# Kernel tuning notes

Hardware: AMD Instinct MI355X
Metric: run time of the kernel (lower is better)

Reference implementation:

```python
import jax, jax.numpy as jnp
import numpy as np

NUM_HEADS = 16


def setup_inputs() -> dict:
    key = jax.random.key(0)
    ks = jax.random.split(key, 7)
    B, S, D = 2, 2048, 1024
    scale = 1.0 / np.sqrt(D)
    return {
        "queries": jax.random.normal(ks[0], (B, S, D), jnp.float32),
        "keys": jax.random.normal(ks[1], (B, S, D), jnp.float32),
        "values": jax.random.normal(ks[2], (B, S, D), jnp.float32),
        "Wq": jax.random.normal(ks[3], (D, D), jnp.float32) * scale,
        "Wk": jax.random.normal(ks[4], (D, D), jnp.float32) * scale,
        "Wv": jax.random.normal(ks[5], (D, D), jnp.float32) * scale,
        "Wo": jax.random.normal(ks[6], (D, D), jnp.float32) * scale,
    }


def _split_heads(x, h):
    # [B, S, D] -> [B, h, S, D/h]
    B, S, D = x.shape
    return x.reshape(B, S, h, D // h).transpose(0, 2, 1, 3)


def reference(queries, keys, values, Wq, Wk, Wv, Wo):
    h = NUM_HEADS
    q = _split_heads(queries @ Wq, h)  # [B, h, S, dh]
    k = _split_heads(keys @ Wk, h)
    v = _split_heads(values @ Wv, h)
    dh = q.shape[-1]
    scores = jnp.einsum("bhqd,bhkd->bhqk", q, k) / jnp.sqrt(jnp.float32(dh))
    attn = jax.nn.softmax(scores, axis=-1)
    y = jnp.einsum("bhqk,bhkd->bhqd", attn, v)  # [B, h, S, dh]
    B, _, S, _ = y.shape
    y = y.transpose(0, 2, 1, 3).reshape(B, S, h * dh)
    return y @ Wo
```

## Files before the change

### kernel.cpp

```cpp
#include <hip/hip_runtime.h>
#include <hip/hip_bf16.h>


typedef __attribute__((ext_vector_type(8))) short bf16x8;
typedef __attribute__((ext_vector_type(4))) float f32x4;
typedef __attribute__((ext_vector_type(16))) float f32x16;
typedef __attribute__((ext_vector_type(4))) unsigned int u32x4;

#define QSCALE 0.18033688011112042f

__device__ __forceinline__ unsigned short f2b(float f) {
    unsigned int u = __float_as_uint(f);
    u += 0x7FFFu + ((u >> 16) & 1u);
    return (unsigned short)(u >> 16);
}

__device__ __forceinline__ unsigned cvt_pk_bf16(float lo, float hi) {
    unsigned r;
    asm("v_cvt_pk_bf16_f32 %0, %1, %2" : "=v"(r) : "v"(lo), "v"(hi));
    return r;
}

__device__ __forceinline__ float exp2a(float x) {
    float r;
    asm("v_exp_f32 %0, %1\n\ts_nop 1" : "=v"(r) : "v"(x));
    return r;
}

__device__ __forceinline__ void gld_lds16(const void* g, void* l) {
    __builtin_amdgcn_global_load_lds(
        (const __attribute__((address_space(1))) unsigned int*)g,
        (__attribute__((address_space(3))) unsigned int*)l, 16, 0, 0);
}

__global__ __launch_bounds__(256) void f32_to_bf16_3(
    const float* __restrict__ i0, const float* __restrict__ i1, const float* __restrict__ i2,
    unsigned short* __restrict__ o0, unsigned short* __restrict__ o1, unsigned short* __restrict__ o2)
{
    const int z = blockIdx.y;
    const float* in = z == 0 ? i0 : (z == 1 ? i1 : i2);
    unsigned short* out = z == 0 ? o0 : (z == 1 ? o1 : o2);
    int i = blockIdx.x * 256 + threadIdx.x;
    float4 v = ((const float4*)in)[i];
    ushort4 o;
    o.x = f2b(v.x); o.y = f2b(v.y); o.z = f2b(v.z); o.w = f2b(v.w);
    ((ushort4*)out)[i] = o;
}

__global__ __launch_bounds__(256) void transpose_w4(
    const float* __restrict__ W0, const float* __restrict__ W1,
    const float* __restrict__ W2, const float* __restrict__ W3,
    unsigned short* __restrict__ O0, unsigned short* __restrict__ O1,
    unsigned short* __restrict__ O2, unsigned short* __restrict__ O3)
{
    __shared__ unsigned short tile[32][33];
    const int z = blockIdx.z;
    const float* in = z == 0 ? W0 : z == 1 ? W1 : z == 2 ? W2 : W3;
    unsigned short* out = z == 0 ? O0 : z == 1 ? O1 : z == 2 ? O2 : O3;
    const int c0 = blockIdx.x * 32, r0 = blockIdx.y * 32;
    const int tx = threadIdx.x, ty = threadIdx.y;
#pragma unroll
    for (int i = 0; i < 4; ++i)
        tile[ty + i * 8][tx] = f2b(in[(size_t)(r0 + ty + i * 8) * 1024 + c0 + tx]);
    __syncthreads();
#pragma unroll
    for (int i = 0; i < 4; ++i)
        out[(size_t)(c0 + ty + i * 8) * 1024 + r0 + tx] = tile[tx][ty + i * 8];
}

template <int BN, int MODE>
__global__ __launch_bounds__(256) void gemm_bt(
    const unsigned short* __restrict__ A0, const unsigned short* __restrict__ A1,
    const unsigned short* __restrict__ A2,
    const unsigned short* __restrict__ B0, const unsigned short* __restrict__ B1,
    const unsigned short* __restrict__ B2,
    void* __restrict__ Cq, void* __restrict__ Ck, void* __restrict__ Cv)
{
    constexpr int K = 1024, N = 1024;
    constexpr int NB = BN / 32;
    __shared__ unsigned short lds_a[128 * 32];
    __shared__ unsigned short lds_b[BN * 32];
    const int tid = threadIdx.x;
    const int wid = tid >> 6, ln = tid & 15, lg = (tid & 63) >> 4;
    const int z = (MODE == 1) ? blockIdx.z : 0;
    const unsigned short* A = (z == 0) ? A0 : (z == 1) ? A1 : A2;
    const unsigned short* Bt = (z == 0) ? B0 : (z == 1) ? B1 : B2;
    const int m0 = blockIdx.y * 128, n0 = blockIdx.x * BN;
    const int wr = wid >> 1, wc = wid & 1;

    f32x4 acc[4][NB];
#pragma unroll
    for (int m = 0; m < 4; ++m)
#pragma unroll
        for (int n = 0; n < NB; ++n) acc[m][n] = {};

    const int srow = tid >> 2, scol = (tid & 3) * 8;
    const unsigned short* ga = A + (size_t)(m0 + srow) * K + scol;
    const unsigned short* gb = Bt + (size_t)(n0 + srow) * K + scol;
    unsigned short* la = lds_a + wid * 512;
    unsigned short* lb = lds_b + wid * 512;

    for (int k0 = 0; k0 < K; k0 += 32) {
        gld_lds16(ga + k0, la);
        gld_lds16(ga + k0 + 64 * K, la + 2048);
        gld_lds16(gb + k0, lb);
        if constexpr (BN == 128) gld_lds16(gb + k0 + 64 * K, lb + 2048);
        __syncthreads();

        bf16x8 af[4], bfr[NB];
#pragma unroll
        for (int m = 0; m < 4; ++m)
            af[m] = *(const bf16x8*)&lds_a[(wr * 64 + m * 16 + ln) * 32 + lg * 8];
#pragma unroll
        for (int n = 0; n < NB; ++n)
            bfr[n] = *(const bf16x8*)&lds_b[(wc * (BN / 2) + n * 16 + ln) * 32 + lg * 8];
#pragma unroll
        for (int m = 0; m < 4; ++m)
#pragma unroll
            for (int n = 0; n < NB; ++n)
                acc[m][n] = __builtin_amdgcn_mfma_f32_16x16x32_bf16(af[m], bfr[n], acc[m][n], 0, 0, 0);
        __syncthreads();
    }

    const int gcb = n0 + wc * (BN / 2) + ln;
    const int grb = m0 + wr * 64 + lg * 4;

    if constexpr (MODE == 0) {
        float* C = (float*)Cq;
#pragma unroll
        for (int m = 0; m < 4; ++m)
#pragma unroll
            for (int n = 0; n < NB; ++n)
#pragma unroll
                for (int r = 0; r < 4; ++r)
                    C[(size_t)(grb + m * 16 + r) * N + gcb + n * 16] = acc[m][n][r];
    } else {
        if (z == 0) {
            unsigned short* C = (unsigned short*)Cq;
#pragma unroll
            for (int m = 0; m < 4; ++m)
#pragma unroll
                for (int n = 0; n < NB; ++n)
#pragma unroll
                    for (int r = 0; r < 4; ++r)
                        C[(size_t)(grb + m * 16 + r) * N + gcb + n * 16] =
                            f2b(acc[m][n][r] * QSCALE);
        } else if (z == 1) {
            unsigned short* Kp = (unsigned short*)Ck;
#pragma unroll
            for (int m = 0; m < 4; ++m)
#pragma unroll
                for (int n = 0; n < NB; ++n) {
                    int gr = grb + m * 16, gc = gcb + n * 16;
                    int bq = gr >> 11, kvg = gr & 2047, kvt = kvg >> 6;
                    int h = gc >> 6, d = gc & 63;
                    size_t img = ((size_t)(bq * 16 + h) * 32 + kvt) * 4096;
                    int ks = d >> 4, hib = (d >> 3) & 1, i = d & 7;
                    int kvb = kvg & 63, T = kvb >> 5;
                    size_t base = img + T * 2048 + ks * 512 + hib * 256 + i;
#pragma unroll
                    for (int r = 0; r < 4; ++r)
                        Kp[base + ((kvb & 31) + r) * 8] = f2b(acc[m][n][r]);
                }
        } else {
            unsigned short* Vp = (unsigned short*)Cv;
#pragma unroll
            for (int m = 0; m < 4; ++m)
#pragma unroll
                for (int n = 0; n < NB; ++n) {
                    int gr = grb + m * 16, gc = gcb + n * 16;
                    int bq = gr >> 11, kvg = gr & 2047, kvt = kvg >> 6;
                    int h = gc >> 6, d = gc & 63;
                    size_t img = ((size_t)(bq * 16 + h) * 32 + kvt) * 4096;
                    int kvb = kvg & 63;
                    int T = kvb >> 5, g = (kvb >> 3) & 3, hib = (kvb >> 2) & 1;
                    int kstep = 2 * T + (g >> 1);
                    int dt = d >> 5, ln31 = d & 31;
                    size_t addr = img + dt * 2048 + kstep * 512 + hib * 256 + ln31 * 8 + (g & 1) * 4;
                    uint2 w;
                    w.x = cvt_pk_bf16(acc[m][n][0], acc[m][n][1]);
                    w.y = cvt_pk_bf16(acc[m][n][2], acc[m][n][3]);
                    *(uint2*)(Vp + addr) = w;
                }
        }
    }
}

__global__ __launch_bounds__(256) void attn_kernel(
    const unsigned short* __restrict__ Qp,
    const unsigned short* __restrict__ Kpack,
    const unsigned short* __restrict__ Vpack,
    unsigned short* __restrict__ Y)
{
    __shared__ unsigned short lds_k[2][4096];
    __shared__ unsigned short lds_v[2][4096];
    const int tid = threadIdx.x;
    const int wid = tid >> 6, lane = tid & 63;
    const int q31 = lane & 31, hi = lane >> 5;

    const int logical = (blockIdx.x & 7) * 64 + (blockIdx.x >> 3);
    const int bx = logical & 15, bh = logical >> 4;
    const int b = bh >> 4, h = bh & 15;
    const int tok0 = b * 2048;
    const int qw = bx * 128 + wid * 32;

    const unsigned short* qrow = Qp + (size_t)(tok0 + qw + q31) * 1024 + h * 64 + hi * 8;
    bf16x8 qf[4];
#pragma unroll
    for (int ks = 0; ks < 4; ++ks) qf[ks] = *(const bf16x8*)(qrow + ks * 16);

    const unsigned short* gk = Kpack + (size_t)bh * (32 * 4096);
    const unsigned short* gv = Vpack + (size_t)bh * (32 * 4096);

    float m_run = -1e30f, l_run = 0.f;
    f32x16 o[2] = {{}, {}};

    auto stage = [&](int buf, int kvt) {
#pragma unroll
        for (int c = 0; c < 2; ++c) {
            int m = c * 4 + wid;
            gld_lds16(gk + (size_t)kvt * 4096 + m * 512 + lane * 8, &lds_k[buf][m * 512]);
            gld_lds16(gv + (size_t)kvt * 4096 + m * 512 + lane * 8, &lds_v[buf][m * 512]);
        }
    };

    stage(0, 0);
    __syncthreads();

    for (int kvt = 0; kvt < 32; ++kvt) {
        const int buf = kvt & 1;
        if (kvt < 31) stage(buf ^ 1, kvt + 1);

        f32x16 st[2];
#pragma unroll
        for (int T = 0; T < 2; ++T) {
            f32x16 zacc = {};
#pragma unroll
            for (int ks = 0; ks < 4; ++ks) {
                bf16x8 ka = *(const bf16x8*)&lds_k[buf][T * 2048 + ks * 512 + lane * 8];
                zacc = __builtin_amdgcn_mfma_f32_32x32x16_bf16(ka, qf[ks], zacc, 0, 0, 0);
            }
            st[T] = zacc;
        }

        float pm = st[0][0];
#pragma unroll
        for (int r = 1; r < 16; ++r) pm = fmaxf(pm, st[0][r]);
#pragma unroll
        for (int r = 0; r < 16; ++r) pm = fmaxf(pm, st[1][r]);
        pm = fmaxf(pm, __shfl_xor(pm, 32));
        const float mn = fmaxf(m_run, pm);
        const float alpha = exp2a(m_run - mn);
        m_run = mn;

        float rs = 0.f;
        unsigned pk[2][8];
#pragma unroll
        for (int T = 0; T < 2; ++T)
#pragma unroll
            for (int g = 0; g < 4; ++g) {
                float p0 = exp2a(st[T][g * 4 + 0] - mn);
                float p1 = exp2a(st[T][g * 4 + 1] - mn);
                float p2 = exp2a(st[T][g * 4 + 2] - mn);
                float p3 = exp2a(st[T][g * 4 + 3] - mn);
                rs += (p0 + p1) + (p2 + p3);
                pk[T][g * 2 + 0] = cvt_pk_bf16(p0, p1);
                pk[T][g * 2 + 1] = cvt_pk_bf16(p2, p3);
            }
        rs += __shfl_xor(rs, 32);
        l_run = l_run * alpha + rs;

#pragma unroll
        for (int r = 0; r < 16; ++r) { o[0][r] *= alpha; o[1][r] *= alpha; }

#pragma unroll
        for (int dt = 0; dt < 2; ++dt)
#pragma unroll
            for (int kstep = 0; kstep < 4; ++kstep) {
                bf16x8 va = *(const bf16x8*)&lds_v[buf][dt * 2048 + kstep * 512 + lane * 8];
                u32x4 w = {pk[kstep >> 1][4 * (kstep & 1) + 0], pk[kstep >> 1][4 * (kstep & 1) + 1],
                           pk[kstep >> 1][4 * (kstep & 1) + 2], pk[kstep >> 1][4 * (kstep & 1) + 3]};
                o[dt] = __builtin_amdgcn_mfma_f32_32x32x16_bf16(
                    va, __builtin_bit_cast(bf16x8, w), o[dt], 0, 0, 0);
            }
        __syncthreads();
    }

    const float inv = __builtin_amdgcn_rcpf(l_run);
    unsigned short* yout = Y + (size_t)(tok0 + qw + q31) * 1024 + h * 64 + hi * 4;
#pragma unroll
    for (int dt = 0; dt < 2; ++dt)
#pragma unroll
        for (int g = 0; g < 4; ++g) {
            uint2 w;
            w.x = cvt_pk_bf16(o[dt][g * 4 + 0] * inv, o[dt][g * 4 + 1] * inv);
            w.y = cvt_pk_bf16(o[dt][g * 4 + 2] * inv, o[dt][g * 4 + 3] * inv);
            *(uint2*)(yout + dt * 32 + g * 8) = w;
        }
}

extern "C" void kernel_launch(void* const* d_in, const int* in_sizes, int n_in,
                              void* d_out, int out_size, void* d_ws, size_t ws_size,
                              hipStream_t stream)
{
    const float* q_f = (const float*)d_in[0];
    const float* k_f = (const float*)d_in[1];
    const float* v_f = (const float*)d_in[2];
    const float* Wq  = (const float*)d_in[3];
    const float* Wk  = (const float*)d_in[4];
    const float* Wv  = (const float*)d_in[5];
    const float* Wo  = (const float*)d_in[6];
    float* out = (float*)d_out;

    const size_t X = (size_t)4096 * 1024;
    const size_t W = (size_t)1024 * 1024;
    unsigned short* ws  = (unsigned short*)d_ws;
    unsigned short* qb  = ws;
    unsigned short* kb  = qb + X;
    unsigned short* vb  = kb + X;
    unsigned short* wqt = vb + X;
    unsigned short* wkt = wqt + W;
    unsigned short* wvt = wkt + W;
    unsigned short* wot = wvt + W;
    unsigned short* Qp  = wot + W;
    unsigned short* Kpk = Qp + X;
    unsigned short* Vpk = Kpk + X;
    unsigned short* Yb  = Vpk + X;

    f32_to_bf16_3<<<dim3(4096, 3), 256, 0, stream>>>(q_f, k_f, v_f, qb, kb, vb);
    transpose_w4<<<dim3(32, 32, 4), dim3(32, 8), 0, stream>>>(Wq, Wk, Wv, Wo,
                                                              wqt, wkt, wvt, wot);
    gemm_bt<128, 1><<<dim3(8, 32, 3), 256, 0, stream>>>(qb, kb, vb, wqt, wkt, wvt,
                                                        Qp, Kpk, Vpk);
    attn_kernel<<<512, 256, 0, stream>>>(Qp, Kpk, Vpk, Yb);
    gemm_bt<64, 0><<<dim3(16, 32, 1), 256, 0, stream>>>(Yb, nullptr, nullptr,
                                                        wot, nullptr, nullptr,
                                                        out, nullptr, nullptr);
}
```

Measured before the change: 249.9 us.

## Double-buffer GEMM LDS tiles and halve attention block size with builtin exp2

The bf16 GEMM now keeps two LDS buffers and issues the global-to-LDS loads for the next K-slice before computing on the current one. This is meant to overlap memory latency with MFMA work, at the cost of twice the LDS footprint. The attention kernel moves from 4 waves per block to 2, covering 64 queries per block over 1024 blocks, so each wave stages more K/V data. The hand-written v_exp_f32 asm with s_nop is replaced by the compiler builtin, which lets the scheduler handle hazards itself.

```diff
diff --git a/kernel.cpp b/kernel.cpp
--- a/kernel.cpp
+++ b/kernel.cpp
@@ -18,12 +18,6 @@
 __device__ __forceinline__ unsigned cvt_pk_bf16(float lo, float hi) {
     unsigned r;
     asm("v_cvt_pk_bf16_f32 %0, %1, %2" : "=v"(r) : "v"(lo), "v"(hi));
-    return r;
-}
-
-__device__ __forceinline__ float exp2a(float x) {
-    float r;
-    asm("v_exp_f32 %0, %1\n\ts_nop 1" : "=v"(r) : "v"(x));
     return r;
 }
 
@@ -78,8 +72,8 @@
 {
     constexpr int K = 1024, N = 1024;
     constexpr int NB = BN / 32;
-    __shared__ unsigned short lds_a[128 * 32];
-    __shared__ unsigned short lds_b[BN * 32];
+    __shared__ unsigned short lds_a[2][128 * 32];
+    __shared__ unsigned short lds_b[2][BN * 32];
     const int tid = threadIdx.x;
     const int wid = tid >> 6, ln = tid & 15, lg = (tid & 63) >> 4;
     const int z = (MODE == 1) ? blockIdx.z : 0;
@@ -94,26 +88,30 @@
 #pragma unroll
         for (int n = 0; n < NB; ++n) acc[m][n] = {};
 
-    const int srow = tid >> 2, scol = (tid & 3) * 8;
-    const unsigned short* ga = A + (size_t)(m0 + srow) * K + scol;
-    const unsigned short* gb = Bt + (size_t)(n0 + srow) * K + scol;
-    unsigned short* la = lds_a + wid * 512;
-    unsigned short* lb = lds_b + wid * 512;
+    const unsigned short* ga = A + (size_t)(m0 + (tid >> 2)) * K + (tid & 3) * 8;
+    const unsigned short* gb = Bt + (size_t)(n0 + (tid >> 2)) * K + (tid & 3) * 8;
+
+    auto stage = [&](int buf, int k0) {
+        gld_lds16(ga + k0, &lds_a[buf][wid * 512]);
+        gld_lds16(ga + k0 + 64 * K, &lds_a[buf][wid * 512 + 2048]);
+        gld_lds16(gb + k0, &lds_b[buf][wid * 512]);
+        if constexpr (BN == 128) gld_lds16(gb + k0 + 64 * K, &lds_b[buf][wid * 512 + 2048]);
+    };
+
+    stage(0, 0);
+    __syncthreads();
 
     for (int k0 = 0; k0 < K; k0 += 32) {
-        gld_lds16(ga + k0, la);
-        gld_lds16(ga + k0 + 64 * K, la + 2048);
-        gld_lds16(gb + k0, lb);
-        if constexpr (BN == 128) gld_lds16(gb + k0 + 64 * K, lb + 2048);
-        __syncthreads();
+        const int buf = (k0 >> 5) & 1;
+        if (k0 + 32 < K) stage(buf ^ 1, k0 + 32);
 
         bf16x8 af[4], bfr[NB];
 #pragma unroll
         for (int m = 0; m < 4; ++m)
-            af[m] = *(const bf16x8*)&lds_a[(wr * 64 + m * 16 + ln) * 32 + lg * 8];
+            af[m] = *(const bf16x8*)&lds_a[buf][(wr * 64 + m * 16 + ln) * 32 + lg * 8];
 #pragma unroll
         for (int n = 0; n < NB; ++n)
-            bfr[n] = *(const bf16x8*)&lds_b[(wc * (BN / 2) + n * 16 + ln) * 32 + lg * 8];
+            bfr[n] = *(const bf16x8*)&lds_b[buf][(wc * (BN / 2) + n * 16 + ln) * 32 + lg * 8];
 #pragma unroll
         for (int m = 0; m < 4; ++m)
 #pragma unroll
@@ -186,7 +184,7 @@
     }
 }
 
-__global__ __launch_bounds__(256) void attn_kernel(
+__global__ __launch_bounds__(128) void attn_kernel(
     const unsigned short* __restrict__ Qp,
     const unsigned short* __restrict__ Kpack,
     const unsigned short* __restrict__ Vpack,
@@ -198,11 +196,11 @@
     const int wid = tid >> 6, lane = tid & 63;
     const int q31 = lane & 31, hi = lane >> 5;
 
-    const int logical = (blockIdx.x & 7) * 64 + (blockIdx.x >> 3);
-    const int bx = logical & 15, bh = logical >> 4;
+    const int logical = (blockIdx.x & 7) * 128 + (blockIdx.x >> 3);
+    const int bx = logical & 31, bh = logical >> 5;
     const int b = bh >> 4, h = bh & 15;
     const int tok0 = b * 2048;
-    const int qw = bx * 128 + wid * 32;
+    const int qw = bx * 64 + wid * 32;
 
     const unsigned short* qrow = Qp + (size_t)(tok0 + qw + q31) * 1024 + h * 64 + hi * 8;
     bf16x8 qf[4];
@@ -217,8 +215,8 @@
 
     auto stage = [&](int buf, int kvt) {
 #pragma unroll
-        for (int c = 0; c < 2; ++c) {
-            int m = c * 4 + wid;
+        for (int c = 0; c < 4; ++c) {
+            int m = c * 2 + wid;
             gld_lds16(gk + (size_t)kvt * 4096 + m * 512 + lane * 8, &lds_k[buf][m * 512]);
             gld_lds16(gv + (size_t)kvt * 4096 + m * 512 + lane * 8, &lds_v[buf][m * 512]);
         }
@@ -250,7 +248,7 @@
         for (int r = 0; r < 16; ++r) pm = fmaxf(pm, st[1][r]);
         pm = fmaxf(pm, __shfl_xor(pm, 32));
         const float mn = fmaxf(m_run, pm);
-        const float alpha = exp2a(m_run - mn);
+        const float alpha = __builtin_amdgcn_exp2f(m_run - mn);
         m_run = mn;
 
         float rs = 0.f;
@@ -259,10 +257,10 @@
         for (int T = 0; T < 2; ++T)
 #pragma unroll
             for (int g = 0; g < 4; ++g) {
-                float p0 = exp2a(st[T][g * 4 + 0] - mn);
-                float p1 = exp2a(st[T][g * 4 + 1] - mn);
-                float p2 = exp2a(st[T][g * 4 + 2] - mn);
-                float p3 = exp2a(st[T][g * 4 + 3] - mn);
+                float p0 = __builtin_amdgcn_exp2f(st[T][g * 4 + 0] - mn);
+                float p1 = __builtin_amdgcn_exp2f(st[T][g * 4 + 1] - mn);
+                float p2 = __builtin_amdgcn_exp2f(st[T][g * 4 + 2] - mn);
+                float p3 = __builtin_amdgcn_exp2f(st[T][g * 4 + 3] - mn);
                 rs += (p0 + p1) + (p2 + p3);
                 pk[T][g * 2 + 0] = cvt_pk_bf16(p0, p1);
                 pk[T][g * 2 + 1] = cvt_pk_bf16(p2, p3);
@@ -332,7 +330,7 @@
                                                               wqt, wkt, wvt, wot);
     gemm_bt<128, 1><<<dim3(8, 32, 3), 256, 0, stream>>>(qb, kb, vb, wqt, wkt, wvt,
                                                         Qp, Kpk, Vpk);
-    attn_kernel<<<512, 256, 0, stream>>>(Qp, Kpk, Vpk, Yb);
+    attn_kernel<<<1024, 128, 0, stream>>>(Qp, Kpk, Vpk, Yb);
     gemm_bt<64, 0><<<dim3(16, 32, 1), 256, 0, stream>>>(Yb, nullptr, nullptr,
                                                         wot, nullptr, nullptr,
                                                         out, nullptr, nullptr);
```

Measured after the change: 238.7 us. 4.5% less time.
